# Kernel tuning notes

Hardware: AMD Instinct MI355X
Metric: run time of the kernel (lower is better)

The kernel has to match this reference:

```python
import jax, jax.numpy as jnp
import numpy as np

NDIM = 3
RADIUS = 0.2
N_POINT = 1024
N_SAMPLE = 32
D_INPUT = 64
D_HIDDEN = [64, 128, 256]
B, N = 8, 16384


def setup_inputs() -> dict:
    key = jax.random.key(0)
    ks = jax.random.split(key, 8)
    xyz = jax.random.uniform(ks[0], (B, NDIM, N), dtype=jnp.float32)
    points = jax.random.normal(ks[1], (B, D_INPUT, N), dtype=jnp.float32)
    # pointwise conv (kernel 1x1) weights: [out, in] plus bias [out]
    c_in = D_INPUT + NDIM
    inp = {"xyz": xyz, "points": points}
    for i, c_out in enumerate(D_HIDDEN):
        scale = 1.0 / np.sqrt(c_in)
        inp[f"w{i}"] = jax.random.uniform(ks[2 + 2 * i], (c_out, c_in), dtype=jnp.float32, minval=-scale, maxval=scale)
        inp[f"b{i}"] = jax.random.uniform(ks[3 + 2 * i], (c_out,), dtype=jnp.float32, minval=-scale, maxval=scale)
        c_in = c_out
    return inp


def farthest_point_sample(xyz):
    # xyz: [B, N, 3] -> idx [B, n_point]; deterministic, first index seeds (fps_method='first')
    b, n, _ = xyz.shape

    def step(carry, _):
        dist, farthest = carry  # [B, N], [B]
        centroid = jnp.take_along_axis(xyz, farthest[:, None, None], axis=1)  # [B,1,3]
        d = jnp.sum((xyz - centroid) ** 2, axis=-1)  # [B,N]
        dist = jnp.minimum(dist, d)
        return (dist, jnp.argmax(dist, axis=-1)), farthest

    init = (jnp.full((b, n), jnp.inf, xyz.dtype), jnp.zeros((b,), jnp.int32))
    _, idx = jax.lax.scan(step, init, None, length=N_POINT)
    return idx.T.astype(jnp.int32)  # [B, n_point]


def ball_query(new_xyz, xyz):
    # new_xyz: [B,S,3], xyz: [B,N,3] -> idx [B,S,K]
    n = xyz.shape[1]
    sqr = jnp.sum((new_xyz[:, :, None, :] - xyz[:, None, :, :]) ** 2, axis=-1)  # [B,S,N]
    cand = jnp.where(sqr > RADIUS * RADIUS, n, jnp.arange(n, dtype=jnp.int32))
    idx = jnp.sort(cand, axis=-1)[:, :, :N_SAMPLE]
    first = idx[:, :, :1]
    return jnp.where(idx == n, first, idx)


def sample_and_group(xyz, points):
    # xyz: [B,N,3], points: [B,N,D]
    fps_idx = farthest_point_sample(xyz)                      # [B,S]
    new_xyz = jax.vmap(lambda a, i: a[i])(xyz, fps_idx)       # [B,S,3]
    idx = jax.lax.stop_gradient(ball_query(jax.lax.stop_gradient(new_xyz), jax.lax.stop_gradient(xyz)))  # [B,S,K]
    grouped_xyz = jax.vmap(lambda a, i: a[i])(xyz, idx)       # [B,S,K,3]
    grouped_xyz_norm = grouped_xyz - new_xyz[:, :, None, :]
    grouped_points = jax.vmap(lambda a, i: a[i])(points, idx) # [B,S,K,D]
    new_points = jnp.concatenate([grouped_xyz_norm, grouped_points], axis=-1)  # [B,S,K,3+D]
    return new_xyz, new_points


def reference(xyz, points, w0, b0, w1, b1, w2, b2):
    # xyz: [B,3,N], points: [B,D,N]
    xyz_t = jnp.transpose(xyz, (0, 2, 1))      # [B,N,3]
    pts_t = jnp.transpose(points, (0, 2, 1))   # [B,N,D]
    _, new_points = sample_and_group(xyz_t, pts_t)      # [B,S,K,C]
    x = jnp.transpose(new_points, (0, 3, 2, 1))          # [B,C,K,S]
    for w, b in ((w0, b0), (w1, b1), (w2, b2)):
        x = jax.nn.silu(jnp.einsum('oc,bcks->boks', w, x) + b[None, :, None, None])
    return jnp.mean(x, axis=2)                            # [B, d_hidden[-1], S]
```

## Files before the change

kernel.cpp:

```cpp
#include <hip/hip_runtime.h>
#include <math.h>

#define NPTS 16384
#define NCTR 1024
#define BATCH 8
#define NCELL 512

typedef unsigned long long u64;
typedef unsigned int u32;

__device__ __forceinline__ float sq_dist(float x, float y, float z,
                                         float cx, float cy, float cz) {
  float dx = __fsub_rn(x, cx);
  float dy = __fsub_rn(y, cy);
  float dz = __fsub_rn(z, cz);
  return __fadd_rn(__fadd_rn(__fmul_rn(dx, dx), __fmul_rn(dy, dy)), __fmul_rn(dz, dz));
}

__device__ __forceinline__ float silu_f(float x) {
  return x / (1.0f + __expf(-x));
}

__device__ __forceinline__ u64 kmax(u64 a, u64 b) { return a > b ? a : b; }

__device__ __forceinline__ int morton_cell(float x, float y, float z) {
  int mx = min(7, max(0, (int)(x * 8.0f)));
  int my = min(7, max(0, (int)(y * 8.0f)));
  int mz = min(7, max(0, (int)(z * 8.0f)));
  int m = 0;
#pragma unroll
  for (int k = 0; k < 3; ++k) {
    m |= ((mx >> k) & 1) << (3 * k + 2);
    m |= ((my >> k) & 1) << (3 * k + 1);
    m |= ((mz >> k) & 1) << (3 * k + 0);
  }
  return m;
}

__global__ __launch_bounds__(1024) void sort_kernel(
    const float* __restrict__ xyz, float* __restrict__ sxg,
    float* __restrict__ syg, float* __restrict__ szg, int* __restrict__ sog) {
  const int b = blockIdx.x, t = threadIdx.x;
  const float* X = xyz + (size_t)b * 3 * NPTS;
  const float* Y = X + NPTS;
  const float* Z = X + 2 * NPTS;
  __shared__ int cnt[NCELL];
  __shared__ int off[NCELL];
  __shared__ int start[NCELL];
  __shared__ int so_l[NPTS];
  for (int e = t; e < NCELL; e += 1024) cnt[e] = 0;
  __syncthreads();
#pragma unroll
  for (int j = 0; j < 16; ++j) {
    const int n = t + (j << 10);
    atomicAdd(&cnt[morton_cell(X[n], Y[n], Z[n])], 1);
  }
  __syncthreads();
  if (t < NCELL) off[t] = cnt[t];
  __syncthreads();
  for (int d = 1; d < NCELL; d <<= 1) {
    int v = 0;
    if (t < NCELL) { v = off[t]; if (t >= d) v += off[t - d]; }
    __syncthreads();
    if (t < NCELL) off[t] = v;
    __syncthreads();
  }
  if (t < NCELL) { off[t] -= cnt[t]; start[t] = off[t]; }
  __syncthreads();
  for (int j = 0; j < 16; ++j) {
    const int n = t + (j << 10);
    const int pos = atomicAdd(&off[morton_cell(X[n], Y[n], Z[n])], 1);
    so_l[pos] = n;
    __syncthreads();
  }
  if (t < NCELL) {
    const int s0 = start[t], k = cnt[t];
    for (int i2 = 1; i2 < k; ++i2) {
      const int key = so_l[s0 + i2];
      int j2 = i2 - 1;
      while (j2 >= 0 && so_l[s0 + j2] > key) {
        so_l[s0 + j2 + 1] = so_l[s0 + j2];
        --j2;
      }
      so_l[s0 + j2 + 1] = key;
    }
  }
  __syncthreads();
  float* sx = sxg + (size_t)b * NPTS;
  float* sy = syg + (size_t)b * NPTS;
  float* sz = szg + (size_t)b * NPTS;
  int* so = sog + (size_t)b * NPTS;
#pragma unroll
  for (int j = 0; j < 16; ++j) {
    const int pos = t + (j << 10);
    const int n = so_l[pos];
    so[pos] = n;
    sx[pos] = X[n];
    sy[pos] = Y[n];
    sz[pos] = Z[n];
  }
}

#define CH_LIST(F) \
  F(0,a0)  F(1,a1)  F(2,a2)  F(3,a3)  F(4,a0)  F(5,a1)  F(6,a2)  F(7,a3)  \
  F(8,a0)  F(9,a1)  F(10,a2) F(11,a3) F(12,a0) F(13,a1) F(14,a2) F(15,a3)

__global__ __launch_bounds__(1024)
void fps_kernel(const float* __restrict__ xyz, const float* __restrict__ sxg,
                const float* __restrict__ syg, const float* __restrict__ szg,
                const int* __restrict__ sog, int* __restrict__ fps_idx) {
  const int b = blockIdx.x;
  const int t = threadIdx.x;
  const int w = t >> 6, lane = t & 63;
  const float* X = xyz + (size_t)b * 3 * NPTS;
  const float* Y = X + NPTS;
  const float* Z = X + 2 * NPTS;
  const float* SX = sxg + (size_t)b * NPTS;
  const float* SY = syg + (size_t)b * NPTS;
  const float* SZ = szg + (size_t)b * NPTS;
  const int* SO = sog + (size_t)b * NPTS;

  __shared__ float sxy[2 * NPTS];
  __shared__ __align__(16) u64 slot[3][2];
  __shared__ float s_zw[3][16];
  __shared__ int fps_lds[NCTR];

#define DECL_CH(c, acc) float z##c, d##c; u32 lo##c;
  CH_LIST(DECL_CH)
#undef DECL_CH

  const int wbase = (w << 6) + lane;

  float bmnx = __builtin_inff(), bmxx = -__builtin_inff();
  float bmny = __builtin_inff(), bmxy = -__builtin_inff();
  float bmnz = __builtin_inff(), bmxz = -__builtin_inff();

#define INIT_CH(c, acc)                                         \
  {                                                             \
    const int p = ((c) << 10) + wbase;                          \
    const float xv = SX[p], yv = SY[p], zv = SZ[p];             \
    sxy[2 * p] = xv; sxy[2 * p + 1] = yv;                       \
    z##c = zv;                                                  \
    const int o = SO[p];                                        \
    lo##c = ((u32)(16383 - o) << 14) | (u32)p;                  \
    d##c = __builtin_inff();                                    \
    float mnx = xv, mxx = xv, mny = yv, mxy = yv;               \
    float mnz = zv, mxz = zv;                                   \
    _Pragma("unroll")                                           \
    for (int off = 32; off >= 1; off >>= 1) {                   \
      mnx = fminf(mnx, __shfl_xor(mnx, off));                   \
      mxx = fmaxf(mxx, __shfl_xor(mxx, off));                   \
      mny = fminf(mny, __shfl_xor(mny, off));                   \
      mxy = fmaxf(mxy, __shfl_xor(mxy, off));                   \
      mnz = fminf(mnz, __shfl_xor(mnz, off));                   \
      mxz = fmaxf(mxz, __shfl_xor(mxz, off));                   \
    }                                                           \
    if (lane == c) {                                            \
      bmnx = mnx; bmxx = mxx; bmny = mny;                       \
      bmxy = mxy; bmnz = mnz; bmxz = mxz;                       \
    }                                                           \
  }
  CH_LIST(INIT_CH)
#undef INIT_CH

#define PIN_CH(c, acc) asm volatile("" : "+v"(z##c));
  CH_LIST(PIN_CH)
#undef PIN_CH

  if (t < 6) slot[t / 2][t & 1] = 0ull;
  if (t == 0) fps_lds[0] = 0;
  __syncthreads();

  float cx = X[0], cy = Y[0], cz = Z[0];
  float gd = __builtin_inff();
  u64 gkey = 0ull;
  float gz = 0.0f;
  int wmaxch = 0;

#define MK(c) ((((u64)__float_as_uint(d##c)) << 32) | (u64)lo##c)
#define KSEL(ka, za, kb, zb, ko, zo)          \
  {                                           \
    const u64 ka_ = (ka), kb_ = (kb);         \
    const bool g_ = ka_ > kb_;                \
    ko = g_ ? ka_ : kb_;                      \
    zo = g_ ? (za) : (zb);                    \
  }

  for (int i = 1; i < NCTR; ++i) {
    const float ux = fmaxf(fmaxf(__fsub_rn(bmnx, cx), __fsub_rn(cx, bmxx)), 0.0f);
    const float uy = fmaxf(fmaxf(__fsub_rn(bmny, cy), __fsub_rn(cy, bmxy)), 0.0f);
    const float uz = fmaxf(fmaxf(__fsub_rn(bmnz, cz), __fsub_rn(cz, bmxz)), 0.0f);
    const float lb = __fadd_rn(__fadd_rn(__fmul_rn(ux, ux), __fmul_rn(uy, uy)),
                               __fmul_rn(uz, uz));
    const u32 mask = (u32)__ballot(!(__fmul_rn(lb, 0.9999f) >= gd));
    if (mask != 0u) {
      if (__builtin_popcount(mask) >= 6) {
#define UPDU_CH(c, acc)                                                  \
        {                                                                \
          const float2 xy =                                              \
              *(const float2*)(sxy + 2 * (((c) << 10) + wbase));         \
          const float dd = sq_dist(xy.x, xy.y, z##c, cx, cy, cz);        \
          d##c = fminf(d##c, dd);                                        \
        }
        CH_LIST(UPDU_CH)
#undef UPDU_CH
      } else {
#define UPDG_CH(c, acc)                                                  \
        if (mask & (1u << (c))) {                                        \
          const float2 xy =                                              \
              *(const float2*)(sxy + 2 * (((c) << 10) + wbase));         \
          float dd = sq_dist(xy.x, xy.y, z##c, cx, cy, cz);              \
          asm volatile("" : "+v"(dd));                                   \
          d##c = fminf(d##c, dd);                                        \
        }
        CH_LIST(UPDG_CH)
#undef UPDG_CH
      }
      if ((mask >> wmaxch) & 1u) {
        u64 m0, m1, m2, m3, m4, m5, m6, m7, q0, q1, q2, q3, h0, h1, kk;
        float n0, n1, n2, n3, n4, n5, n6, n7, r0, r1, r2, r3, e0, e1, bz;
        KSEL(MK(0), z0, MK(1), z1, m0, n0)    KSEL(MK(2), z2, MK(3), z3, m1, n1)
        KSEL(MK(4), z4, MK(5), z5, m2, n2)    KSEL(MK(6), z6, MK(7), z7, m3, n3)
        KSEL(MK(8), z8, MK(9), z9, m4, n4)    KSEL(MK(10), z10, MK(11), z11, m5, n5)
        KSEL(MK(12), z12, MK(13), z13, m6, n6) KSEL(MK(14), z14, MK(15), z15, m7, n7)
        KSEL(m0, n0, m1, n1, q0, r0)  KSEL(m2, n2, m3, n3, q1, r1)
        KSEL(m4, n4, m5, n5, q2, r2)  KSEL(m6, n6, m7, n7, q3, r3)
        KSEL(q0, r0, q1, r1, h0, e0)  KSEL(q2, r2, q3, r3, h1, e1)
        KSEL(h0, e0, h1, e1, kk, bz)
#pragma unroll
        for (int off = 32; off >= 1; off >>= 1) {
          const u64 ok = __shfl_xor(kk, off);
          const float oz = __shfl_xor(bz, off);
          const bool g_ = ok > kk;
          kk = g_ ? ok : kk;
          bz = g_ ? oz : bz;
        }
        gkey = kk;
        gz = bz;
        gd = __uint_as_float((u32)(gkey >> 32));
        wmaxch = (int)(((u32)gkey >> 10) & 15u);
      }
    }
    const int si = i % 3;
    if (lane == 0) {
      s_zw[si][w] = gz;
      atomicMax(&slot[si][w & 1], gkey);
    }
    if (t == 0) {
      const int nsi = si == 2 ? 0 : si + 1;
      slot[nsi][0] = 0ull;
      slot[nsi][1] = 0ull;
    }
    __syncthreads();

    const u64 m = kmax(slot[si][0], slot[si][1]);
    const u32 lowb = (u32)m;
    const int pw = (int)(lowb & 0x3FFFu);
    if (t == 0) fps_lds[i] = 16383 - (int)((lowb >> 14) & 0x3FFFu);

    const int pu = __builtin_amdgcn_readfirstlane(pw);
    const float2 cxy = *(const float2*)(sxy + 2 * pu);
    cx = cxy.x;
    cy = cxy.y;
    cz = s_zw[si][(pu >> 6) & 15];
  }
#undef MK
#undef KSEL

  __syncthreads();
  for (int e = t; e < NCTR; e += 1024) fps_idx[b * NCTR + e] = fps_lds[e];
}

__global__ __launch_bounds__(256) void ballq_kernel(const float* __restrict__ xyz,
                                                    const int* __restrict__ fps_idx,
                                                    int* __restrict__ ball_idx) {
  const int gw = (blockIdx.x * 256 + threadIdx.x) >> 6;
  const int lane = threadIdx.x & 63;
  const int b = gw >> 10;
  const float* X = xyz + (size_t)b * 3 * NPTS;
  const float* Y = X + NPTS;
  const float* Z = X + 2 * NPTS;
  const int c = fps_idx[gw];
  const float cx = X[c], cy = Y[c], cz = Z[c];
  int* out = ball_idx + (size_t)gw * 32;
  const float R2 = 0.04f;

  int cnt = 0, first = -1;
  for (int base = 0; base < NPTS; base += 64) {
    const int j = base + lane;
    const float d = sq_dist(X[j], Y[j], Z[j], cx, cy, cz);
    const bool inb = !(d > R2);
    const unsigned long long m = __ballot(inb);
    if (first < 0 && m != 0ull) first = base + __ffsll(m) - 1;
    if (inb) {
      const int pos = cnt + __popcll(m & ((1ull << lane) - 1ull));
      if (pos < 32) out[pos] = j;
    }
    cnt += __popcll(m);
    if (cnt >= 32) break;
  }
  for (int k = cnt + lane; k < 32; k += 64) out[k] = first;
}

__global__ __launch_bounds__(256) void transpose_w_kernel(
    const float* __restrict__ w0, const float* __restrict__ w1,
    const float* __restrict__ w2, float* __restrict__ wt0,
    float* __restrict__ wt1, float* __restrict__ wt2) {
  const int t0 = blockIdx.x * 256 + threadIdx.x;
  const int stride = gridDim.x * 256;
  for (int e = t0; e < 64 * 67; e += stride) {
    int o = e / 67, c = e - o * 67;
    wt0[c * 64 + o] = w0[e];
  }
  for (int e = t0; e < 128 * 64; e += stride) {
    int o = e >> 6, c = e & 63;
    wt1[c * 128 + o] = w1[e];
  }
  for (int e = t0; e < 256 * 128; e += stride) {
    int o = e >> 7, c = e & 127;
    wt2[c * 256 + o] = w2[e];
  }
}

__global__ __launch_bounds__(256, 2) void mlp_kernel(
    const float* __restrict__ xyz, const float* __restrict__ points,
    const int* __restrict__ fps_idx, const int* __restrict__ ball_idx,
    const float* __restrict__ wt0, const float* __restrict__ b0,
    const float* __restrict__ wt1, const float* __restrict__ b1,
    const float* __restrict__ wt2, const float* __restrict__ b2,
    float* __restrict__ out) {
  const int bx = blockIdx.x, b = blockIdx.y, t = threadIdx.x;
  const int s = (bx & 7) * 128 + (bx >> 3);

  __shared__ float A1[64 * 36];
  __shared__ float A2[128 * 36];
  __shared__ float S[8704];
  __shared__ float bias_sh[256];
  __shared__ int jidx[32];
  __shared__ float ctr[3];

  const int g = b * NCTR + s;

  if (t < 32) jidx[t] = ball_idx[(size_t)g * 32 + t];
  if (t < 3) ctr[t] = xyz[((size_t)b * 3 + t) * NPTS + fps_idx[g]];
  float* A0 = S;
  float* Wt0 = S + 67 * 36;
  for (int e = t; e < 67 * 64; e += 256) {
    int c = e >> 6, o = e & 63;
    Wt0[c * 68 + o] = wt0[e];
  }
  if (t < 64) bias_sh[t] = b0[t];
  __syncthreads();

  for (int e = t; e < 67 * 32; e += 256) {
    int c = e >> 5, k = e & 31;
    int j = jidx[k];
    float v;
    if (c < 3)
      v = xyz[((size_t)b * 3 + c) * NPTS + j] - ctr[c];
    else
      v = points[((size_t)b * 64 + (c - 3)) * NPTS + j];
    A0[c * 36 + k] = v;
  }
  __syncthreads();

  {
    const int o0 = (t & 31) * 2;
    const int k0 = (t >> 5) * 4;
    float acc[4][2] = {{0.f, 0.f}, {0.f, 0.f}, {0.f, 0.f}, {0.f, 0.f}};
    for (int c = 0; c < 67; ++c) {
      const float4 a = *(const float4*)(A0 + c * 36 + k0);
      const float2 wv = *(const float2*)(Wt0 + c * 68 + o0);
      acc[0][0] = fmaf(a.x, wv.x, acc[0][0]);
      acc[1][0] = fmaf(a.y, wv.x, acc[1][0]);
      acc[2][0] = fmaf(a.z, wv.x, acc[2][0]);
      acc[3][0] = fmaf(a.w, wv.x, acc[3][0]);
      acc[0][1] = fmaf(a.x, wv.y, acc[0][1]);
      acc[1][1] = fmaf(a.y, wv.y, acc[1][1]);
      acc[2][1] = fmaf(a.z, wv.y, acc[2][1]);
      acc[3][1] = fmaf(a.w, wv.y, acc[3][1]);
    }
#pragma unroll
    for (int i = 0; i < 2; ++i) {
      const float bb = bias_sh[o0 + i];
      float4 r;
      r.x = silu_f(acc[0][i] + bb);
      r.y = silu_f(acc[1][i] + bb);
      r.z = silu_f(acc[2][i] + bb);
      r.w = silu_f(acc[3][i] + bb);
      *(float4*)(A1 + (o0 + i) * 36 + k0) = r;
    }
  }
  __syncthreads();

  float* Wt1 = S;
  for (int e = t; e < 128 * 64; e += 256) {
    int c = e >> 7, o = e & 127;
    Wt1[c * 132 + o] = wt1[e];
  }
  if (t < 128) bias_sh[t] = b1[t];
  __syncthreads();

  {
    const int o0 = (t & 31) * 4;
    const int k0 = (t >> 5) * 4;
    float acc[4][4];
#pragma unroll
    for (int kk = 0; kk < 4; ++kk)
#pragma unroll
      for (int oo = 0; oo < 4; ++oo) acc[kk][oo] = 0.f;
    for (int c = 0; c < 64; ++c) {
      const float4 a = *(const float4*)(A1 + c * 36 + k0);
      const float4 w = *(const float4*)(Wt1 + c * 132 + o0);
      const float av[4] = {a.x, a.y, a.z, a.w};
      const float wv[4] = {w.x, w.y, w.z, w.w};
#pragma unroll
      for (int kk = 0; kk < 4; ++kk)
#pragma unroll
        for (int oo = 0; oo < 4; ++oo)
          acc[kk][oo] = fmaf(av[kk], wv[oo], acc[kk][oo]);
    }
#pragma unroll
    for (int oo = 0; oo < 4; ++oo) {
      const float bb = bias_sh[o0 + oo];
      float4 r;
      r.x = silu_f(acc[0][oo] + bb);
      r.y = silu_f(acc[1][oo] + bb);
      r.z = silu_f(acc[2][oo] + bb);
      r.w = silu_f(acc[3][oo] + bb);
      *(float4*)(A2 + (o0 + oo) * 36 + k0) = r;
    }
  }
  __syncthreads();

  float* Wt2 = S;
  float* P = A1;
  const int o0 = (t & 31) * 2;
  const int k0 = (t >> 5) * 4;
  const int kg = t >> 5;
  for (int chunk = 0; chunk < 4; ++chunk) {
    for (int e = t; e < 64 * 128; e += 256) {
      int c = e >> 6, o = e & 63;
      Wt2[c * 68 + o] = wt2[c * 256 + chunk * 64 + o];
    }
    if (t < 64) bias_sh[t] = b2[chunk * 64 + t];
    __syncthreads();

    float acc[4][2] = {{0.f, 0.f}, {0.f, 0.f}, {0.f, 0.f}, {0.f, 0.f}};
    for (int c = 0; c < 128; ++c) {
      const float4 a = *(const float4*)(A2 + c * 36 + k0);
      const float2 wv = *(const float2*)(Wt2 + c * 68 + o0);
      acc[0][0] = fmaf(a.x, wv.x, acc[0][0]);
      acc[1][0] = fmaf(a.y, wv.x, acc[1][0]);
      acc[2][0] = fmaf(a.z, wv.x, acc[2][0]);
      acc[3][0] = fmaf(a.w, wv.x, acc[3][0]);
      acc[0][1] = fmaf(a.x, wv.y, acc[0][1]);
      acc[1][1] = fmaf(a.y, wv.y, acc[1][1]);
      acc[2][1] = fmaf(a.z, wv.y, acc[2][1]);
      acc[3][1] = fmaf(a.w, wv.y, acc[3][1]);
    }
#pragma unroll
    for (int i = 0; i < 2; ++i) {
      const float bb = bias_sh[o0 + i];
      float sum = silu_f(acc[0][i] + bb) + silu_f(acc[1][i] + bb) +
                  silu_f(acc[2][i] + bb) + silu_f(acc[3][i] + bb);
      P[(o0 + i) * 9 + kg] = sum;
    }
    __syncthreads();
    if (t < 64) {
      float tot = 0.f;
#pragma unroll
      for (int q = 0; q < 8; ++q) tot += P[t * 9 + q];
      out[((size_t)b * 256 + chunk * 64 + t) * NCTR + s] = tot * (1.0f / 32.0f);
    }
    __syncthreads();
  }
}

extern "C" void kernel_launch(void* const* d_in, const int* in_sizes, int n_in,
                              void* d_out, int out_size, void* d_ws, size_t ws_size,
                              hipStream_t stream) {
  const float* xyz = (const float*)d_in[0];
  const float* points = (const float*)d_in[1];
  const float* w0 = (const float*)d_in[2];
  const float* b0 = (const float*)d_in[3];
  const float* w1 = (const float*)d_in[4];
  const float* b1 = (const float*)d_in[5];
  const float* w2 = (const float*)d_in[6];
  const float* b2 = (const float*)d_in[7];
  float* out = (float*)d_out;

  int* fps = (int*)d_ws;
  int* bidx = (int*)d_ws + 8192;
  float* wt0 = (float*)d_ws + 270336;
  float* wt1 = wt0 + 67 * 64;
  float* wt2 = wt1 + 64 * 128;
  float* sxg = (float*)d_ws + 315584;
  float* syg = sxg + BATCH * NPTS;
  float* szg = syg + BATCH * NPTS;
  int* sog = (int*)(szg + BATCH * NPTS);

  transpose_w_kernel<<<64, 256, 0, stream>>>(w0, w1, w2, wt0, wt1, wt2);
  sort_kernel<<<BATCH, 1024, 0, stream>>>(xyz, sxg, syg, szg, sog);
  fps_kernel<<<BATCH, 1024, 0, stream>>>(xyz, sxg, syg, szg, sog, fps);
  ballq_kernel<<<2048, 256, 0, stream>>>(xyz, fps, bidx);
  mlp_kernel<<<dim3(NCTR, BATCH), 256, 0, stream>>>(xyz, points, fps, bidx,
                                                    wt0, b0, wt1, b1, wt2, b2, out);
}
```

Before: 1.872 ms.

## Fuse FPS, ball query and MLP into cooperative producer-consumer mega kernel

Replaces the separate fps, ball-query and MLP launches with one cooperative kernel. Eight blocks run farthest point sampling and publish progress counters every 64 centroids, while 240 consumer blocks spin on those counters and run ball query plus the three-layer MLP for each centroid as soon as it is available. The aim is to hide the downstream work behind the long serial FPS. The risks are that consumer blocks compete with the FPS blocks for CU resources, that a consumer now runs its MLP with 1024 threads per centroid, and that the fallback path is used if the cooperative launch fails.

Measured after the change: 3.961 ms. 2.12x slower.

```diff
diff --git a/kernel.cpp b/kernel.cpp
--- a/kernel.cpp
+++ b/kernel.cpp
@@ -5,6 +5,8 @@
 #define NCTR 1024
 #define BATCH 8
 #define NCELL 512
+#define NCONS 240
+#define GRID_MEGA (BATCH + NCONS)
 
 typedef unsigned long long u64;
 typedef unsigned int u32;
@@ -101,9 +103,348 @@
   }
 }
 
+__global__ __launch_bounds__(256) void transpose_w_kernel(
+    const float* __restrict__ w0, const float* __restrict__ w1,
+    const float* __restrict__ w2, float* __restrict__ wt0,
+    float* __restrict__ wt1, float* __restrict__ wt2,
+    u32* __restrict__ progress) {
+  const int t0 = blockIdx.x * 256 + threadIdx.x;
+  if (t0 < BATCH) progress[t0] = 0u;
+  const int stride = gridDim.x * 256;
+  for (int e = t0; e < 64 * 67; e += stride) {
+    int o = e / 67, c = e - o * 67;
+    wt0[c * 64 + o] = w0[e];
+  }
+  for (int e = t0; e < 128 * 64; e += stride) {
+    int o = e >> 6, c = e & 63;
+    wt1[c * 128 + o] = w1[e];
+  }
+  for (int e = t0; e < 256 * 128; e += stride) {
+    int o = e >> 7, c = e & 127;
+    wt2[c * 256 + o] = w2[e];
+  }
+}
+
 #define CH_LIST(F) \
   F(0,a0)  F(1,a1)  F(2,a2)  F(3,a3)  F(4,a0)  F(5,a1)  F(6,a2)  F(7,a3)  \
   F(8,a0)  F(9,a1)  F(10,a2) F(11,a3) F(12,a0) F(13,a1) F(14,a2) F(15,a3)
+
+union __align__(16) MegaSmem {
+  struct {
+    float sxy[2 * NPTS];
+    u64 slot[3][2];
+    float s_zw[3][16];
+    int fps_lds[NCTR];
+  } p;
+  struct {
+    float A0[67 * 36];
+    float A1[64 * 36];
+    float A2[128 * 36];
+    int jidx[32];
+    float ctr[3];
+  } c;
+};
+
+__global__ __launch_bounds__(1024)
+void mega_kernel(const float* __restrict__ xyz, const float* __restrict__ points,
+                 const float* __restrict__ sxg, const float* __restrict__ syg,
+                 const float* __restrict__ szg, const int* __restrict__ sog,
+                 int* __restrict__ fps_g, u32* __restrict__ progress,
+                 const float* __restrict__ wt0, const float* __restrict__ b0,
+                 const float* __restrict__ wt1, const float* __restrict__ b1,
+                 const float* __restrict__ wt2, const float* __restrict__ b2,
+                 float* __restrict__ out) {
+  __shared__ MegaSmem sm;
+  const int t = threadIdx.x;
+
+  if (blockIdx.x < BATCH) {
+    const int b = blockIdx.x;
+    const int w = t >> 6, lane = t & 63;
+    const float* X = xyz + (size_t)b * 3 * NPTS;
+    const float* Y = X + NPTS;
+    const float* Z = X + 2 * NPTS;
+    const float* SX = sxg + (size_t)b * NPTS;
+    const float* SY = syg + (size_t)b * NPTS;
+    const float* SZ = szg + (size_t)b * NPTS;
+    const int* SO = sog + (size_t)b * NPTS;
+
+#define DECL_CH(c, acc) float z##c, d##c; u32 lo##c;
+    CH_LIST(DECL_CH)
+#undef DECL_CH
+
+    const int wbase = (w << 6) + lane;
+
+    float bmnx = __builtin_inff(), bmxx = -__builtin_inff();
+    float bmny = __builtin_inff(), bmxy = -__builtin_inff();
+    float bmnz = __builtin_inff(), bmxz = -__builtin_inff();
+
+#define INIT_CH(c, acc)                                         \
+    {                                                           \
+      const int p = ((c) << 10) + wbase;                        \
+      const float xv = SX[p], yv = SY[p], zv = SZ[p];           \
+      sm.p.sxy[2 * p] = xv; sm.p.sxy[2 * p + 1] = yv;           \
+      z##c = zv;                                                \
+      const int o = SO[p];                                      \
+      lo##c = ((u32)(16383 - o) << 14) | (u32)p;                \
+      d##c = __builtin_inff();                                  \
+      float mnx = xv, mxx = xv, mny = yv, mxy = yv;             \
+      float mnz = zv, mxz = zv;                                 \
+      _Pragma("unroll")                                         \
+      for (int off = 32; off >= 1; off >>= 1) {                 \
+        mnx = fminf(mnx, __shfl_xor(mnx, off));                 \
+        mxx = fmaxf(mxx, __shfl_xor(mxx, off));                 \
+        mny = fminf(mny, __shfl_xor(mny, off));                 \
+        mxy = fmaxf(mxy, __shfl_xor(mxy, off));                 \
+        mnz = fminf(mnz, __shfl_xor(mnz, off));                 \
+        mxz = fmaxf(mxz, __shfl_xor(mxz, off));                 \
+      }                                                         \
+      if (lane == c) {                                          \
+        bmnx = mnx; bmxx = mxx; bmny = mny;                     \
+        bmxy = mxy; bmnz = mnz; bmxz = mxz;                     \
+      }                                                         \
+    }
+    CH_LIST(INIT_CH)
+#undef INIT_CH
+
+#define PIN_CH(c, acc) asm volatile("" : "+v"(z##c));
+    CH_LIST(PIN_CH)
+#undef PIN_CH
+
+    if (t < 6) sm.p.slot[t / 2][t & 1] = 0ull;
+    if (t == 0) sm.p.fps_lds[0] = 0;
+    __syncthreads();
+
+    float cx = X[0], cy = Y[0], cz = Z[0];
+    float gd = __builtin_inff();
+    u64 gkey = 0ull;
+    float gz = 0.0f;
+    int wmaxch = 0;
+
+#define MK(c) ((((u64)__float_as_uint(d##c)) << 32) | (u64)lo##c)
+#define KSEL(ka, za, kb, zb, ko, zo)          \
+    {                                         \
+      const u64 ka_ = (ka), kb_ = (kb);       \
+      const bool g_ = ka_ > kb_;              \
+      ko = g_ ? ka_ : kb_;                    \
+      zo = g_ ? (za) : (zb);                  \
+    }
+
+    for (int i = 1; i < NCTR; ++i) {
+      const float ux = fmaxf(fmaxf(__fsub_rn(bmnx, cx), __fsub_rn(cx, bmxx)), 0.0f);
+      const float uy = fmaxf(fmaxf(__fsub_rn(bmny, cy), __fsub_rn(cy, bmxy)), 0.0f);
+      const float uz = fmaxf(fmaxf(__fsub_rn(bmnz, cz), __fsub_rn(cz, bmxz)), 0.0f);
+      const float lb = __fadd_rn(__fadd_rn(__fmul_rn(ux, ux), __fmul_rn(uy, uy)),
+                                 __fmul_rn(uz, uz));
+      const u32 mask = (u32)__ballot(!(__fmul_rn(lb, 0.9999f) >= gd));
+      if (mask != 0u) {
+        if (__builtin_popcount(mask) >= 6) {
+#define UPDU_CH(c, acc)                                                    \
+          {                                                                \
+            const float2 xy =                                              \
+                *(const float2*)(sm.p.sxy + 2 * (((c) << 10) + wbase));    \
+            const float dd = sq_dist(xy.x, xy.y, z##c, cx, cy, cz);        \
+            d##c = fminf(d##c, dd);                                        \
+          }
+          CH_LIST(UPDU_CH)
+#undef UPDU_CH
+        } else {
+#define UPDG_CH(c, acc)                                                    \
+          if (mask & (1u << (c))) {                                        \
+            const float2 xy =                                              \
+                *(const float2*)(sm.p.sxy + 2 * (((c) << 10) + wbase));    \
+            float dd = sq_dist(xy.x, xy.y, z##c, cx, cy, cz);              \
+            asm volatile("" : "+v"(dd));                                   \
+            d##c = fminf(d##c, dd);                                        \
+          }
+          CH_LIST(UPDG_CH)
+#undef UPDG_CH
+        }
+        if ((mask >> wmaxch) & 1u) {
+          u64 m0, m1, m2, m3, m4, m5, m6, m7, q0, q1, q2, q3, h0, h1, kk;
+          float n0, n1, n2, n3, n4, n5, n6, n7, r0, r1, r2, r3, e0, e1, bz;
+          KSEL(MK(0), z0, MK(1), z1, m0, n0)    KSEL(MK(2), z2, MK(3), z3, m1, n1)
+          KSEL(MK(4), z4, MK(5), z5, m2, n2)    KSEL(MK(6), z6, MK(7), z7, m3, n3)
+          KSEL(MK(8), z8, MK(9), z9, m4, n4)    KSEL(MK(10), z10, MK(11), z11, m5, n5)
+          KSEL(MK(12), z12, MK(13), z13, m6, n6) KSEL(MK(14), z14, MK(15), z15, m7, n7)
+          KSEL(m0, n0, m1, n1, q0, r0)  KSEL(m2, n2, m3, n3, q1, r1)
+          KSEL(m4, n4, m5, n5, q2, r2)  KSEL(m6, n6, m7, n7, q3, r3)
+          KSEL(q0, r0, q1, r1, h0, e0)  KSEL(q2, r2, q3, r3, h1, e1)
+          KSEL(h0, e0, h1, e1, kk, bz)
+#pragma unroll
+          for (int off = 32; off >= 1; off >>= 1) {
+            const u64 ok = __shfl_xor(kk, off);
+            const float oz = __shfl_xor(bz, off);
+            const bool g_ = ok > kk;
+            kk = g_ ? ok : kk;
+            bz = g_ ? oz : bz;
+          }
+          gkey = kk;
+          gz = bz;
+          gd = __uint_as_float((u32)(gkey >> 32));
+          wmaxch = (int)(((u32)gkey >> 10) & 15u);
+        }
+      }
+      const int si = i % 3;
+      if (lane == 0) {
+        sm.p.s_zw[si][w] = gz;
+        atomicMax(&sm.p.slot[si][w & 1], gkey);
+      }
+      if (t == 0) {
+        const int nsi = si == 2 ? 0 : si + 1;
+        sm.p.slot[nsi][0] = 0ull;
+        sm.p.slot[nsi][1] = 0ull;
+      }
+      __syncthreads();
+
+      const u64 m = kmax(sm.p.slot[si][0], sm.p.slot[si][1]);
+      const u32 lowb = (u32)m;
+      const int pw = (int)(lowb & 0x3FFFu);
+      if (t == 0) sm.p.fps_lds[i] = 16383 - (int)((lowb >> 14) & 0x3FFFu);
+
+      const int pu = __builtin_amdgcn_readfirstlane(pw);
+      const float2 cxy = *(const float2*)(sm.p.sxy + 2 * pu);
+      cx = cxy.x;
+      cy = cxy.y;
+      cz = sm.p.s_zw[si][(pu >> 6) & 15];
+
+      if (w == 0 && (i & 63) == 63) {
+        const int base0 = i - 63;
+        fps_g[b * NCTR + base0 + lane] = sm.p.fps_lds[base0 + lane];
+        if (lane == 0)
+          __hip_atomic_store(&progress[b], (u32)(i + 1), __ATOMIC_RELEASE,
+                             __HIP_MEMORY_SCOPE_AGENT);
+      }
+    }
+#undef MK
+#undef KSEL
+    return;
+  }
+
+  const int cb = blockIdx.x - BATCH;
+  for (int j = cb; j < BATCH * NCTR; j += NCONS) {
+    const int s = j >> 3, b_ = j & 7;
+    if (t == 0) {
+      while (__hip_atomic_load(&progress[b_], __ATOMIC_ACQUIRE,
+                               __HIP_MEMORY_SCOPE_AGENT) < (u32)(s + 1))
+        __builtin_amdgcn_s_sleep(64);
+    }
+    __syncthreads();
+
+    const float* X = xyz + (size_t)b_ * 3 * NPTS;
+    const float* Y = X + NPTS;
+    const float* Z = X + 2 * NPTS;
+
+    if (t < 64) {
+      const int lane = t;
+      const int c = fps_g[b_ * NCTR + s];
+      const float cx = X[c], cy = Y[c], cz = Z[c];
+      if (lane == 0) { sm.c.ctr[0] = cx; sm.c.ctr[1] = cy; sm.c.ctr[2] = cz; }
+      const float R2 = 0.04f;
+      int cnt = 0, first = -1;
+      for (int base = 0; base < NPTS; base += 64) {
+        const int jj = base + lane;
+        const float d = sq_dist(X[jj], Y[jj], Z[jj], cx, cy, cz);
+        const bool inb = !(d > R2);
+        const unsigned long long mm = __ballot(inb);
+        if (first < 0 && mm != 0ull) first = base + __ffsll(mm) - 1;
+        if (inb) {
+          const int pos = cnt + __popcll(mm & ((1ull << lane) - 1ull));
+          if (pos < 32) sm.c.jidx[pos] = jj;
+        }
+        cnt += __popcll(mm);
+        if (cnt >= 32) break;
+      }
+      for (int k2 = cnt + lane; k2 < 32; k2 += 64) sm.c.jidx[k2] = first;
+    }
+    __syncthreads();
+
+    for (int e = t; e < 67 * 32; e += 1024) {
+      int c = e >> 5, k = e & 31;
+      int jj = sm.c.jidx[k];
+      float v;
+      if (c < 3)
+        v = xyz[((size_t)b_ * 3 + c) * NPTS + jj] - sm.c.ctr[c];
+      else
+        v = points[((size_t)b_ * 64 + (c - 3)) * NPTS + jj];
+      sm.c.A0[c * 36 + k] = v;
+    }
+    __syncthreads();
+
+    if (t < 512) {
+      const int o = t & 63, k0 = (t >> 6) * 4;
+      const float bb = b0[o];
+      float a0 = 0.f, a1 = 0.f, a2 = 0.f, a3 = 0.f;
+      for (int c = 0; c < 67; ++c) {
+        const float4 a = *(const float4*)(sm.c.A0 + c * 36 + k0);
+        const float wv = wt0[c * 64 + o];
+        a0 = fmaf(a.x, wv, a0);
+        a1 = fmaf(a.y, wv, a1);
+        a2 = fmaf(a.z, wv, a2);
+        a3 = fmaf(a.w, wv, a3);
+      }
+      float4 r;
+      r.x = silu_f(a0 + bb);
+      r.y = silu_f(a1 + bb);
+      r.z = silu_f(a2 + bb);
+      r.w = silu_f(a3 + bb);
+      *(float4*)(sm.c.A1 + o * 36 + k0) = r;
+    }
+    __syncthreads();
+
+    {
+      const int o = t & 127, k0 = (t >> 7) * 4;
+      const float bb = b1[o];
+      float a0 = 0.f, a1 = 0.f, a2 = 0.f, a3 = 0.f;
+      for (int c = 0; c < 64; ++c) {
+        const float4 a = *(const float4*)(sm.c.A1 + c * 36 + k0);
+        const float wv = wt1[c * 128 + o];
+        a0 = fmaf(a.x, wv, a0);
+        a1 = fmaf(a.y, wv, a1);
+        a2 = fmaf(a.z, wv, a2);
+        a3 = fmaf(a.w, wv, a3);
+      }
+      float4 r;
+      r.x = silu_f(a0 + bb);
+      r.y = silu_f(a1 + bb);
+      r.z = silu_f(a2 + bb);
+      r.w = silu_f(a3 + bb);
+      *(float4*)(sm.c.A2 + o * 36 + k0) = r;
+    }
+    __syncthreads();
+
+    {
+      float* P = sm.c.A1;
+      const int o = t & 127, kg = t >> 7, k0 = kg * 4;
+#pragma unroll
+      for (int half = 0; half < 2; ++half) {
+        const int oo = half * 128 + o;
+        const float bb = b2[oo];
+        float a0 = 0.f, a1 = 0.f, a2 = 0.f, a3 = 0.f;
+        for (int c = 0; c < 128; ++c) {
+          const float4 a = *(const float4*)(sm.c.A2 + c * 36 + k0);
+          const float wv = wt2[c * 256 + oo];
+          a0 = fmaf(a.x, wv, a0);
+          a1 = fmaf(a.y, wv, a1);
+          a2 = fmaf(a.z, wv, a2);
+          a3 = fmaf(a.w, wv, a3);
+        }
+        const float sum = silu_f(a0 + bb) + silu_f(a1 + bb) +
+                          silu_f(a2 + bb) + silu_f(a3 + bb);
+        P[oo * 9 + kg] = sum;
+      }
+    }
+    __syncthreads();
+
+    if (t < 256) {
+      const float* P = sm.c.A1;
+      float tot = 0.f;
+#pragma unroll
+      for (int q = 0; q < 8; ++q) tot += P[t * 9 + q];
+      out[((size_t)b_ * 256 + t) * NCTR + s] = tot * (1.0f / 32.0f);
+    }
+    __syncthreads();
+  }
+}
 
 __global__ __launch_bounds__(1024)
 void fps_kernel(const float* __restrict__ xyz, const float* __restrict__ sxg,
@@ -302,26 +643,6 @@
   for (int k = cnt + lane; k < 32; k += 64) out[k] = first;
 }
 
-__global__ __launch_bounds__(256) void transpose_w_kernel(
-    const float* __restrict__ w0, const float* __restrict__ w1,
-    const float* __restrict__ w2, float* __restrict__ wt0,
-    float* __restrict__ wt1, float* __restrict__ wt2) {
-  const int t0 = blockIdx.x * 256 + threadIdx.x;
-  const int stride = gridDim.x * 256;
-  for (int e = t0; e < 64 * 67; e += stride) {
-    int o = e / 67, c = e - o * 67;
-    wt0[c * 64 + o] = w0[e];
-  }
-  for (int e = t0; e < 128 * 64; e += stride) {
-    int o = e >> 6, c = e & 63;
-    wt1[c * 128 + o] = w1[e];
-  }
-  for (int e = t0; e < 256 * 128; e += stride) {
-    int o = e >> 7, c = e & 127;
-    wt2[c * 256 + o] = w2[e];
-  }
-}
-
 __global__ __launch_bounds__(256, 2) void mlp_kernel(
     const float* __restrict__ xyz, const float* __restrict__ points,
     const int* __restrict__ fps_idx, const int* __restrict__ ball_idx,
@@ -492,6 +813,7 @@
 
   int* fps = (int*)d_ws;
   int* bidx = (int*)d_ws + 8192;
+  u32* progress = (u32*)bidx;
   float* wt0 = (float*)d_ws + 270336;
   float* wt1 = wt0 + 67 * 64;
   float* wt2 = wt1 + 64 * 128;
@@ -500,10 +822,20 @@
   float* szg = syg + BATCH * NPTS;
   int* sog = (int*)(szg + BATCH * NPTS);
 
-  transpose_w_kernel<<<64, 256, 0, stream>>>(w0, w1, w2, wt0, wt1, wt2);
+  transpose_w_kernel<<<64, 256, 0, stream>>>(w0, w1, w2, wt0, wt1, wt2, progress);
   sort_kernel<<<BATCH, 1024, 0, stream>>>(xyz, sxg, syg, szg, sog);
-  fps_kernel<<<BATCH, 1024, 0, stream>>>(xyz, sxg, syg, szg, sog, fps);
-  ballq_kernel<<<2048, 256, 0, stream>>>(xyz, fps, bidx);
-  mlp_kernel<<<dim3(NCTR, BATCH), 256, 0, stream>>>(xyz, points, fps, bidx,
-                                                    wt0, b0, wt1, b1, wt2, b2, out);
-}
+
+  void* args[] = {(void*)&xyz, (void*)&points, (void*)&sxg, (void*)&syg,
+                  (void*)&szg, (void*)&sog, (void*)&fps, (void*)&progress,
+                  (void*)&wt0, (void*)&b0, (void*)&wt1, (void*)&b1,
+                  (void*)&wt2, (void*)&b2, (void*)&out};
+  hipError_t err = hipLaunchCooperativeKernel(
+      reinterpret_cast<const void*>(mega_kernel), dim3(GRID_MEGA), dim3(1024),
+      args, 0, stream);
+  if (err != hipSuccess) {
+    fps_kernel<<<BATCH, 1024, 0, stream>>>(xyz, sxg, syg, szg, sog, fps);
+    ballq_kernel<<<2048, 256, 0, stream>>>(xyz, fps, bidx);
+    mlp_kernel<<<dim3(NCTR, BATCH), 256, 0, stream>>>(xyz, points, fps, bidx,
+                                                      wt0, b0, wt1, b1, wt2, b2, out);
+  }
+}
```
